# Performance work log

Hardware: AMD Instinct MI355X
Metric: run time of the kernel (lower is better)

## Reference

```python
import jax, jax.numpy as jnp
import numpy as np
import math

# ShiftedL2Loss constants derived from init kwargs
SAMPLE_RATE = 48000
ALPHA = 100.0
MAX_DIST = 1.5
DIST_SAMPLES = int(SAMPLE_RATE * MAX_DIST / 340)  # 211
T_WIN = 2 ** int(math.floor(math.log(DIST_SAMPLES, 2)))  # t = 128
S_SHIFTS = T_WIN * 2 + 1                                  # S = 257
T_BIG = T_WIN + S_SHIFTS - 1                              # T = 384
DT = T_WIN                                                # dT = t


def _blackman_window(M):
    # torch.blackman_window(M, periodic=False)
    n = jnp.arange(M, dtype=jnp.float32)
    denom = jnp.float32(M - 1)
    return (0.42 - 0.5 * jnp.cos(2.0 * jnp.pi * n / denom)
            + 0.08 * jnp.cos(4.0 * jnp.pi * n / denom))


def setup_inputs() -> dict:
    key = jax.random.key(0)
    k1, k2 = jax.random.split(key)
    B, C, L = 4, 8, 15104  # L = 118 * 128 -> exact tiling
    data = jax.random.normal(k1, (B, C, L), dtype=jnp.float32)
    target = jax.random.normal(k2, (B, C, L), dtype=jnp.float32)
    return {"data": data, "target": target}


def reference(data, target):
    t, S = T_WIN, S_SHIFTS
    w = ALPHA * (1.0 - _blackman_window(S))  # (S,)

    # flatten to (BC, L)
    x = data.reshape(-1, data.shape[-1])
    r = target.reshape(-1, target.shape[-1])
    L = x.shape[-1]
    N = (L - t) // DT + 1
    Ltrim = (N - 1) * DT + t
    x = x[:, :Ltrim]
    r = r[:, :Ltrim]

    # magnitude normalization on the center region
    d = x[:, t:-t]
    rc = r[:, t:-t]
    d = d - jnp.mean(d, axis=1, keepdims=True)
    rc = rc - jnp.mean(rc, axis=1, keepdims=True)
    mag_x = jnp.sqrt(jnp.mean(d ** 2, axis=1, keepdims=True))
    mag_r = jnp.sqrt(jnp.mean(rc ** 2, axis=1, keepdims=True))
    mag_min = jnp.minimum(mag_x, mag_r)
    mag_norm = jnp.sqrt(mag_min * mag_r) + 0.001  # (BC, 1)
    x = x / mag_norm
    r = r / mag_norm

    # zero-pad reference by t on both sides
    r_pad = jnp.pad(r, ((0, 0), (t, t)))  # (BC, Ltrim + 2t)

    # non-overlapping predicted windows: (BC, N, t)
    xw = x.reshape(-1, N, t)

    # shifted reference windows: (BC, N, S, t)
    starts = (jnp.arange(N) * DT)[:, None, None]
    idx = starts + jnp.arange(S)[None, :, None] + jnp.arange(t)[None, None, :]
    yw = r_pad[:, idx]  # gather -> (BC, N, S, t)

    # per-shift MSE over the window: (BC, N, S)
    mse = jnp.mean((xw[:, :, None, :] - yw) ** 2, axis=-1)

    # shift-weighted penalty, min over shifts, mean over everything
    loss = (mse + 1.0) * (w[None, None, :] + 1.0) - 1.0
    loss = jnp.amin(loss, axis=-1)  # (BC, N)
    return jnp.mean(loss).reshape(1)
```

## Files before the change

### kernel.cpp

```cpp
#include <hip/hip_runtime.h>
#include <math.h>

#define ROWS 32
#define LROW 15104
#define TWIN 128
#define NWIN 118
#define TRIM 14848
#define NW   (ROWS * NWIN)
#define WPB  16
#define BPR  8
#define NBLK (ROWS * BPR)
#define YPAN ((WPB + 2) * TWIN)

__device__ __forceinline__ void window_corr(
        const float* __restrict__ xw,
        const float* __restrict__ yw,
        int lane, int lz,
        float c[4], float sy[4], float& sx_l, float& part_l) {
    {
        float xa = xw[lane], xb = xw[lane + 64];
        float ya = yw[256 + lane], yb = yw[320 + lane];
        float d0 = xa - ya, d1 = xb - yb;
        part_l = d0 * d0 + d1 * d1;
        sx_l   = xa * xa + xb * xb;
    }

    const float4* ys4 = (const float4*)yw;

    float4 yv0 = ys4[lane];
    float yf0 = yv0.x, yf1 = yv0.y, yf2 = yv0.z;
    float c0 = 0.f, c1 = 0.f, c2 = 0.f, c3 = 0.f;
    float q = 0.f;

    #pragma unroll
    for (int kb = 0; kb < 32; ++kb) {
        float4 xv  = *(const float4*)(xw + 4 * kb + lz);
        float4 yv1 = ys4[lane + kb + 1];
        c0 += xv.x*yv0.x + xv.y*yv0.y + xv.z*yv0.z + xv.w*yv0.w;
        c1 += xv.x*yv0.y + xv.y*yv0.z + xv.z*yv0.w + xv.w*yv1.x;
        c2 += xv.x*yv0.z + xv.y*yv0.w + xv.z*yv1.x + xv.w*yv1.y;
        c3 += xv.x*yv0.w + xv.y*yv1.x + xv.z*yv1.y + xv.w*yv1.z;
        q  += yv0.x*yv0.x + yv0.y*yv0.y + yv0.z*yv0.z + yv0.w*yv0.w;
        yv0 = yv1;
    }
    c[0] = c0; c[1] = c1; c[2] = c2; c[3] = c3;
    sy[0] = q;
    sy[1] = sy[0] - yf0*yf0 + yv0.x*yv0.x;
    sy[2] = sy[1] - yf1*yf1 + yv0.y*yv0.y;
    sy[3] = sy[2] - yf2*yf2 + yv0.z*yv0.z;
}

__global__ __launch_bounds__(512) void loss_fused(
        const float* __restrict__ data,
        const float* __restrict__ target,
        float* __restrict__ blocksums) {
    int b0 = blockIdx.x;
    int b  = (b0 & 7) * (NBLK / 8) + (b0 >> 3);
    int row = b / BPR;
    int n0  = (b % BPR) * WPB;
    int tid  = threadIdx.x;
    int wave = tid >> 6;
    int lane = tid & 63;

    int lz;
    asm volatile("v_mov_b32 %0, 0" : "=v"(lz));

    __shared__ float  ys[YPAN];
    __shared__ float4 wsum[8];
    __shared__ float  wl[8];

    const float* xrow = data   + row * LROW;
    const float* rrow = target + row * LROW;

    float sd = 0.f, sd2 = 0.f, sr = 0.f, sr2 = 0.f;
    {
        const float4* x4 = (const float4*)(xrow + TWIN);
        const float4* r4 = (const float4*)(rrow + TWIN);
        for (int i = tid; i < TRIM / 4; i += 512) {
            float4 a = x4[i], bv = r4[i];
            sd  += a.x + a.y + a.z + a.w;
            sd2 += a.x*a.x + a.y*a.y + a.z*a.z + a.w*a.w;
            sr  += bv.x + bv.y + bv.z + bv.w;
            sr2 += bv.x*bv.x + bv.y*bv.y + bv.z*bv.z + bv.w*bv.w;
        }
        #pragma unroll
        for (int off = 32; off > 0; off >>= 1) {
            sd  += __shfl_xor(sd,  off, 64);
            sd2 += __shfl_xor(sd2, off, 64);
            sr  += __shfl_xor(sr,  off, 64);
            sr2 += __shfl_xor(sr2, off, 64);
        }
        if (lane == 0) wsum[wave] = make_float4(sd, sd2, sr, sr2);
    }

    for (int j = tid; j < YPAN / 4; j += 512) {
        int g = (n0 - 1) * TWIN + 4 * j;
        float4 v = make_float4(0.f, 0.f, 0.f, 0.f);
        if (g >= 0 && g < LROW) v = *(const float4*)(rrow + g);
        *(float4*)&ys[4 * j] = v;
    }
    __syncthreads();

    float scale2;
    {
        float td = 0.f, td2 = 0.f, tr = 0.f, tr2 = 0.f;
        #pragma unroll
        for (int i = 0; i < 8; ++i) {
            float4 p = wsum[i];
            td += p.x; td2 += p.y; tr += p.z; tr2 += p.w;
        }
        const float inv = 1.0f / (float)TRIM;
        float md = td * inv, mr = tr * inv;
        float vx = fmaxf(td2 * inv - md * md, 0.f);
        float vr = fmaxf(tr2 * inv - mr * mr, 0.f);
        float mag_x = sqrtf(vx), mag_r = sqrtf(vr);
        float mag_min = fminf(mag_x, mag_r);
        float scale = 1.0f / (sqrtf(mag_min * mag_r) + 0.001f);
        scale2 = scale * scale;
    }

    int  nA     = n0 + wave;
    int  nB     = n0 + 8 + wave;
    bool validA = (nA < NWIN);
    bool validB = (nB < NWIN);
    int  nuA    = __builtin_amdgcn_readfirstlane(validA ? nA : NWIN - 1);
    int  nuB    = __builtin_amdgcn_readfirstlane(validB ? nB : NWIN - 1);

    float cA[4], syA[4], sxA, partA;
    float cB[4], syB[4], sxB, partB;
    window_corr(xrow + nuA * TWIN, ys + wave * TWIN,       lane, lz,
                cA, syA, sxA, partA);
    window_corr(xrow + nuB * TWIN, ys + (wave + 8) * TWIN, lane, lz,
                cB, syB, sxB, partB);

    #pragma unroll
    for (int off = 32; off > 0; off >>= 1) {
        sxA   += __shfl_xor(sxA,   off, 64);
        partA += __shfl_xor(partA, off, 64);
        sxB   += __shfl_xor(sxB,   off, 64);
        partB += __shfl_xor(partB, off, 64);
    }

    const float inv = 1.0f / (float)TWIN;
    int   s0  = lane * 4;
    float wp[4];
    #pragma unroll
    for (int j = 0; j < 4; ++j) {
        float ph = (float)(s0 + j) * (float)(M_PI / 128.0);
        float cp = __cosf(ph);
        float bw = 0.42f - 0.5f*cp + 0.08f*(2.f*cp*cp - 1.f);
        wp[j] = 100.f * (1.f - bw) + 1.f;
    }

    float lminA = 1e30f, lminB = 1e30f;
    #pragma unroll
    for (int j = 0; j < 4; ++j) {
        float mA = scale2 * (sxA - 2.f*cA[j] + syA[j]) * inv;
        float mB = scale2 * (sxB - 2.f*cB[j] + syB[j]) * inv;
        lminA = fminf(lminA, (mA + 1.f) * wp[j] - 1.f);
        lminB = fminf(lminB, (mB + 1.f) * wp[j] - 1.f);
    }
    lminA = fminf(lminA, (scale2 * partA * inv + 1.f) * 101.f - 1.f);
    lminB = fminf(lminB, (scale2 * partB * inv + 1.f) * 101.f - 1.f);

    #pragma unroll
    for (int off = 32; off > 0; off >>= 1) {
        lminA = fminf(lminA, __shfl_xor(lminA, off, 64));
        lminB = fminf(lminB, __shfl_xor(lminB, off, 64));
    }

    float wsum_loss = (validA ? lminA : 0.f) + (validB ? lminB : 0.f);

    if (lane == 0) wl[wave] = wsum_loss;
    __syncthreads();
    if (tid == 0) {
        float s = 0.f;
        #pragma unroll
        for (int i = 0; i < 8; ++i) s += wl[i];
        blocksums[b] = s;
    }
}

__global__ __launch_bounds__(256) void finish_kernel(
        const float* __restrict__ blocksums,
        float* __restrict__ out) {
    int tid = threadIdx.x;
    float s = 0.f;
    for (int i = tid; i < NBLK; i += 256) s += blocksums[i];
    __shared__ float sh[256];
    sh[tid] = s;
    __syncthreads();
    for (int off = 128; off > 0; off >>= 1) {
        if (tid < off) sh[tid] += sh[tid + off];
        __syncthreads();
    }
    if (tid == 0) out[0] = sh[0] / (float)NW;
}

extern "C" void kernel_launch(void* const* d_in, const int* in_sizes, int n_in,
                              void* d_out, int out_size, void* d_ws, size_t ws_size,
                              hipStream_t stream) {
    const float* data   = (const float*)d_in[0];
    const float* target = (const float*)d_in[1];
    float* blocksums = (float*)d_ws;

    loss_fused<<<NBLK, 512, 0, stream>>>(data, target, blocksums);
    finish_kernel<<<1, 256, 0, stream>>>(blocksums, (float*)d_out);
}
```

Before: 15.76 us.

## Stage per-wave private reference segments and compute correlations before block barrier

Each wave now loads its own 384-float reference segment per window into a private LDS slice, so the correlation math can run before the block-wide barrier, overlapping with the row statistics reduction. This removes the shared panel load plus barrier that sat before the correlation work. In exchange, reference data is loaded redundantly (three times the shared panel) and LDS usage grows to about 24KB per block. Correctness relies on wave-local LDS visibility without a barrier, which holds within a single wavefront.

```diff
diff --git a/kernel.cpp b/kernel.cpp
--- a/kernel.cpp
+++ b/kernel.cpp
@@ -10,7 +10,7 @@
 #define WPB  16
 #define BPR  8
 #define NBLK (ROWS * BPR)
-#define YPAN ((WPB + 2) * TWIN)
+#define YSEG 768
 
 __device__ __forceinline__ void window_corr(
         const float* __restrict__ xw,
@@ -48,6 +48,24 @@
     sy[1] = sy[0] - yf0*yf0 + yv0.x*yv0.x;
     sy[2] = sy[1] - yf1*yf1 + yv0.y*yv0.y;
     sy[3] = sy[2] - yf2*yf2 + yv0.z*yv0.z;
+}
+
+__device__ __forceinline__ void stage_window(
+        const float* __restrict__ rrow, int n, float* __restrict__ seg,
+        int lane) {
+    int base = (n - 1) * TWIN;
+    {
+        int g = base + 4 * lane;
+        float4 v = make_float4(0.f, 0.f, 0.f, 0.f);
+        if (g >= 0 && g < LROW) v = *(const float4*)(rrow + g);
+        *(float4*)&seg[4 * lane] = v;
+    }
+    if (lane < 32) {
+        int g = base + 4 * (lane + 64);
+        float4 v = make_float4(0.f, 0.f, 0.f, 0.f);
+        if (g >= 0 && g < LROW) v = *(const float4*)(rrow + g);
+        *(float4*)&seg[4 * (lane + 64)] = v;
+    }
 }
 
 __global__ __launch_bounds__(512) void loss_fused(
@@ -65,17 +83,42 @@
     int lz;
     asm volatile("v_mov_b32 %0, 0" : "=v"(lz));
 
-    __shared__ float  ys[YPAN];
+    __shared__ float  ys[8][YSEG];
     __shared__ float4 wsum[8];
     __shared__ float  wl[8];
 
     const float* xrow = data   + row * LROW;
     const float* rrow = target + row * LROW;
 
-    float sd = 0.f, sd2 = 0.f, sr = 0.f, sr2 = 0.f;
+    int  nA     = n0 + wave;
+    int  nB     = n0 + 8 + wave;
+    bool validA = (nA < NWIN);
+    bool validB = (nB < NWIN);
+    int  nuA    = __builtin_amdgcn_readfirstlane(validA ? nA : NWIN - 1);
+    int  nuB    = __builtin_amdgcn_readfirstlane(validB ? nB : NWIN - 1);
+
+    float* segA = &ys[wave][0];
+    float* segB = &ys[wave][384];
+    stage_window(rrow, nuA, segA, lane);
+    stage_window(rrow, nuB, segB, lane);
+
+    float cA[4], syA[4], sxA, partA;
+    float cB[4], syB[4], sxB, partB;
+    window_corr(xrow + nuA * TWIN, segA, lane, lz, cA, syA, sxA, partA);
+    window_corr(xrow + nuB * TWIN, segB, lane, lz, cB, syB, sxB, partB);
+
+    #pragma unroll
+    for (int off = 32; off > 0; off >>= 1) {
+        sxA   += __shfl_xor(sxA,   off, 64);
+        partA += __shfl_xor(partA, off, 64);
+        sxB   += __shfl_xor(sxB,   off, 64);
+        partB += __shfl_xor(partB, off, 64);
+    }
+
     {
         const float4* x4 = (const float4*)(xrow + TWIN);
         const float4* r4 = (const float4*)(rrow + TWIN);
+        float sd = 0.f, sd2 = 0.f, sr = 0.f, sr2 = 0.f;
         for (int i = tid; i < TRIM / 4; i += 512) {
             float4 a = x4[i], bv = r4[i];
             sd  += a.x + a.y + a.z + a.w;
@@ -92,13 +135,6 @@
         }
         if (lane == 0) wsum[wave] = make_float4(sd, sd2, sr, sr2);
     }
-
-    for (int j = tid; j < YPAN / 4; j += 512) {
-        int g = (n0 - 1) * TWIN + 4 * j;
-        float4 v = make_float4(0.f, 0.f, 0.f, 0.f);
-        if (g >= 0 && g < LROW) v = *(const float4*)(rrow + g);
-        *(float4*)&ys[4 * j] = v;
-    }
     __syncthreads();
 
     float scale2;
@@ -119,28 +155,6 @@
         scale2 = scale * scale;
     }
 
-    int  nA     = n0 + wave;
-    int  nB     = n0 + 8 + wave;
-    bool validA = (nA < NWIN);
-    bool validB = (nB < NWIN);
-    int  nuA    = __builtin_amdgcn_readfirstlane(validA ? nA : NWIN - 1);
-    int  nuB    = __builtin_amdgcn_readfirstlane(validB ? nB : NWIN - 1);
-
-    float cA[4], syA[4], sxA, partA;
-    float cB[4], syB[4], sxB, partB;
-    window_corr(xrow + nuA * TWIN, ys + wave * TWIN,       lane, lz,
-                cA, syA, sxA, partA);
-    window_corr(xrow + nuB * TWIN, ys + (wave + 8) * TWIN, lane, lz,
-                cB, syB, sxB, partB);
-
-    #pragma unroll
-    for (int off = 32; off > 0; off >>= 1) {
-        sxA   += __shfl_xor(sxA,   off, 64);
-        partA += __shfl_xor(partA, off, 64);
-        sxB   += __shfl_xor(sxB,   off, 64);
-        partB += __shfl_xor(partB, off, 64);
-    }
-
     const float inv = 1.0f / (float)TWIN;
     int   s0  = lane * 4;
     float wp[4];
```

New measurement: 59.45 us. 277% more time.
